# Performance work log

Hardware: AMD Instinct MI355X
Metric: run time of the kernel (lower is better)

The kernel has to match this reference:

```python
import jax, jax.numpy as jnp
import numpy as np

B, S, D_IN, D_OUT, H = 2, 2048, 1024, 1024, 16
DH = D_OUT // H


def setup_inputs() -> dict:
    key = jax.random.key(0)
    ks = jax.random.split(key, 6)
    sd_in = 1.0 / np.sqrt(D_IN)
    sd_out = 1.0 / np.sqrt(D_OUT)
    return {
        "x": jax.random.normal(ks[0], (B, S, D_IN), dtype=jnp.float32),
        "Wq": jax.random.uniform(ks[1], (D_IN, D_OUT), jnp.float32, -sd_in, sd_in),
        "Wk": jax.random.uniform(ks[2], (D_IN, D_OUT), jnp.float32, -sd_in, sd_in),
        "Wv": jax.random.uniform(ks[3], (D_IN, D_OUT), jnp.float32, -sd_in, sd_in),
        "Wo": jax.random.uniform(ks[4], (D_OUT, D_OUT), jnp.float32, -sd_out, sd_out),
        "bo": jax.random.uniform(ks[5], (D_OUT,), jnp.float32, -sd_out, sd_out),
    }


def reference(x, Wq, Wk, Wv, Wo, bo):
    b, n, _ = x.shape
    dh = DH
    # project and split heads: [b, n, d_out] -> [b, H, n, dh]
    def split(t):
        return t.reshape(b, n, H, dh).transpose(0, 2, 1, 3)
    q = split(x @ Wq)
    k = split(x @ Wk)
    v = split(x @ Wv)
    scores = jnp.einsum("bhqd,bhkd->bhqk", q, k)  # [b, H, n, n]
    causal = jnp.triu(jnp.ones((n, n), dtype=bool), k=1)
    scores = jnp.where(causal, -jnp.inf, scores)
    # NOTE: source scales by sqrt(num_tokens), not sqrt(d_head) — faithful.
    scale = 1.0 / (n ** 0.5)
    attn = jax.nn.softmax(scores * scale, axis=-1)
    ctx = jnp.einsum("bhqk,bhkd->bhqd", attn, v)  # [b, H, n, dh]
    ctx = ctx.transpose(0, 2, 1, 3).reshape(b, n, H * dh)
    return ctx @ Wo + bo
```

## Files before the change

### kernel.cpp

```cpp
#include <hip/hip_runtime.h>
#include <hip/hip_bf16.h>
#include <stdint.h>

#define B_   2
#define S_   2048
#define DIN  1024
#define DOUT 1024
#define H_   16
#define DH_  64

typedef __bf16 bf16_t;
typedef bf16_t bf16x8 __attribute__((ext_vector_type(8)));
typedef float  f32x4  __attribute__((ext_vector_type(4)));

#define WAITV(n) asm volatile("s_waitcnt vmcnt(" #n ")" ::: "memory")

static __device__ __forceinline__ void gld_lds16(const void* g, void* l) {
  __builtin_amdgcn_global_load_lds((const __attribute__((address_space(1))) void*)g,
                                   (__attribute__((address_space(3))) void*)l, 16, 0, 0);
}

static __device__ __forceinline__ unsigned short f2bf(float f) {
  __hip_bfloat16 h = __float2bfloat16(f);
  return __builtin_bit_cast(unsigned short, h);
}

static __device__ __forceinline__ float fexp2(float x) {
#if __has_builtin(__builtin_amdgcn_exp2f)
  return __builtin_amdgcn_exp2f(x);
#else
  return exp2f(x);
#endif
}

__global__ __launch_bounds__(256) void k_convert_x(const float* __restrict__ x,
                                                   unsigned short* __restrict__ xb) {
  int i = (blockIdx.x * 256 + threadIdx.x) * 4;
  float4 v = *reinterpret_cast<const float4*>(x + i);
  ushort4 o;
  o.x = f2bf(v.x); o.y = f2bf(v.y); o.z = f2bf(v.z); o.w = f2bf(v.w);
  *reinterpret_cast<ushort4*>(xb + i) = o;
}

__global__ __launch_bounds__(256) void k_transpose_w(const float* __restrict__ Wq,
                                                     const float* __restrict__ Wk,
                                                     const float* __restrict__ Wv,
                                                     const float* __restrict__ Wo,
                                                     __hip_bfloat16* __restrict__ Wt3,
                                                     __hip_bfloat16* __restrict__ Wot) {
  __shared__ float tile[32][33];
  const int z = blockIdx.z;
  const float* src = (z == 0) ? Wq : (z == 1) ? Wk : (z == 2) ? Wv : Wo;
  __hip_bfloat16* dst = (z < 3) ? (Wt3 + (size_t)z * DIN * DOUT) : Wot;
  const int n0 = blockIdx.x * 32, k0 = blockIdx.y * 32;
  const int tx = threadIdx.x, ty = threadIdx.y;
  #pragma unroll
  for (int i = ty; i < 32; i += 8)
    tile[i][tx] = src[(size_t)(k0 + i) * DOUT + n0 + tx];
  __syncthreads();
  #pragma unroll
  for (int i = ty; i < 32; i += 8)
    dst[(size_t)(n0 + i) * DIN + k0 + tx] = __float2bfloat16(tile[tx][i]);
}

template <int MODE, int TN>
__global__ __launch_bounds__(256) void k_gemm_bt(
    const __hip_bfloat16* __restrict__ A,
    const __hip_bfloat16* __restrict__ Bt,
    __hip_bfloat16* __restrict__ Qb, __hip_bfloat16* __restrict__ Kb,
    __hip_bfloat16* __restrict__ Vtb,
    float* __restrict__ Out, const float* __restrict__ bias,
    int M, int N, int K)
{
  constexpr int NFRAG = TN / 32;
  constexpr int LPT = 2 + TN / 64;
  __shared__ __align__(16) __hip_bfloat16 As[3][128 * 32];
  __shared__ __align__(16) __hip_bfloat16 Bs[3][TN * 32];
  const int tid = threadIdx.x;
  const int lane = tid & 63, wid = tid >> 6;
  const int r15 = lane & 15, g = lane >> 4;
  const int m0 = blockIdx.x * 128, n0 = blockIdx.y * TN;
  const int wr = wid >> 1, wc = wid & 1;
  f32x4 acc[4][NFRAG] = {};

  auto stage = [&](int bi, int kt) {
    #pragma unroll
    for (int i = 0; i < 2; ++i) {
      const int c = i * 256 + tid;
      const int row = c >> 2, kb = (c & 3) * 8;
      gld_lds16(A + (size_t)(m0 + row) * K + kt + kb, (void*)(As[bi] + (size_t)(c & ~63) * 8));
    }
    if constexpr (TN == 128) {
      #pragma unroll
      for (int i = 0; i < 2; ++i) {
        const int c = i * 256 + tid;
        const int row = c >> 2, kb = (c & 3) * 8;
        gld_lds16(Bt + (size_t)(n0 + row) * K + kt + kb, (void*)(Bs[bi] + (size_t)(c & ~63) * 8));
      }
    } else {
      const int c = tid;
      const int row = c >> 2, kb = (c & 3) * 8;
      gld_lds16(Bt + (size_t)(n0 + row) * K + kt + kb, (void*)(Bs[bi] + (size_t)(c & ~63) * 8));
    }
  };

  const int NT = K >> 5;
  stage(0, 0); stage(1, 32);
  if constexpr (TN == 128) WAITV(4); else WAITV(3);
  __builtin_amdgcn_s_barrier();

  int bi = 0;
  for (int t = 0; t < NT; ++t) {
    int bs = bi + 2; if (bs >= 3) bs -= 3;
    const bool st = (t + 2 < NT);
    if (st) stage(bs, (t + 2) * 32);
    bf16x8 af[4], bfr[NFRAG];
    #pragma unroll
    for (int mi = 0; mi < 4; ++mi)
      af[mi] = *reinterpret_cast<const bf16x8*>(As[bi] + (wr * 64 + mi * 16 + r15) * 32 + g * 8);
    #pragma unroll
    for (int ni = 0; ni < NFRAG; ++ni)
      bfr[ni] = *reinterpret_cast<const bf16x8*>(Bs[bi] + (wc * (TN / 2) + ni * 16 + r15) * 32 + g * 8);
    __builtin_amdgcn_s_setprio(1);
    #pragma unroll
    for (int mi = 0; mi < 4; ++mi)
      #pragma unroll
      for (int ni = 0; ni < NFRAG; ++ni)
        acc[mi][ni] = __builtin_amdgcn_mfma_f32_16x16x32_bf16(af[mi], bfr[ni], acc[mi][ni], 0, 0, 0);
    __builtin_amdgcn_s_setprio(0);
    if (t + 1 < NT) {
      if (st) { if constexpr (TN == 128) WAITV(4); else WAITV(3); }
      else    { WAITV(0); }
      __builtin_amdgcn_s_barrier();
    }
    bi = (bi + 1 == 3) ? 0 : bi + 1;
  }

  #pragma unroll
  for (int mi = 0; mi < 4; ++mi) {
    #pragma unroll
    for (int ni = 0; ni < NFRAG; ++ni) {
      const int mb = m0 + wr * 64 + mi * 16 + g * 4;
      const int n  = n0 + wc * (TN / 2) + ni * 16 + r15;
      if (MODE == 0) {
        const int w = n >> 10, nn = n & 1023;
        const int h = nn >> 6, dh = nn & 63;
        const int b = mb >> 11, s = mb & 2047;
        const size_t bh = (size_t)(b * H_ + h);
        if (w == 2) {
          ushort4 pv;
          pv.x = f2bf(acc[mi][ni][0]); pv.y = f2bf(acc[mi][ni][1]);
          pv.z = f2bf(acc[mi][ni][2]); pv.w = f2bf(acc[mi][ni][3]);
          *reinterpret_cast<ushort4*>((unsigned short*)Vtb + (bh * DH_ + dh) * S_ + s) = pv;
        } else {
          #pragma unroll
          for (int rr = 0; rr < 4; ++rr) {
            float v = acc[mi][ni][rr];
            if (w == 0) v *= 0.022097086912079608f * 1.4426950408889634f;
            const __hip_bfloat16 hv = __float2bfloat16(v);
            if (w == 0) Qb[(bh * S_ + s + rr) * DH_ + dh] = hv;
            else        Kb[(bh * S_ + s + rr) * DH_ + dh] = hv;
          }
        }
      } else {
        #pragma unroll
        for (int rr = 0; rr < 4; ++rr)
          Out[(size_t)(mb + rr) * N + n] = acc[mi][ni][rr] + bias[n];
      }
    }
  }
}

__global__ __launch_bounds__(256) void k_attn(
    const __hip_bfloat16* __restrict__ Qb,
    const __hip_bfloat16* __restrict__ Kb,
    const __hip_bfloat16* __restrict__ Vtb,
    __hip_bfloat16* __restrict__ Ctx)
{
  __shared__ __align__(16) __hip_bfloat16 Ks[2][64 * 64];
  __shared__ __align__(16) __hip_bfloat16 Vs[2][64 * 64];
  __shared__ __align__(16) unsigned short Pl[4][16 * 64];
  const int tid = threadIdx.x, lane = tid & 63, w = tid >> 6;
  const int r15 = lane & 15, g = lane >> 4;
  const int bh = blockIdx.x;
  const int b = bh >> 4, h = bh & 15;
  const int qb = 31 - blockIdx.y;
  const __hip_bfloat16* Qh = Qb  + (size_t)bh * S_ * DH_;
  const __hip_bfloat16* Kh = Kb  + (size_t)bh * S_ * DH_;
  const __hip_bfloat16* Vh = Vtb + (size_t)bh * DH_ * S_;
  char* PlW = (char*)&Pl[w][0];
  const int sw = (r15 & 7);
  const float FIXM = 4.0f;

  auto stage = [&](int bufi, int t) {
    const int kv0 = t * 64;
    #pragma unroll
    for (int i = 0; i < 2; ++i) {
      const int c = i * 256 + tid;
      const int r = c >> 3;
      const int scc = (c & 7) ^ (r & 7);
      const int cbase = i * 256 + w * 64;
      gld_lds16(Kh + (size_t)(kv0 + r) * DH_ + scc * 8, (void*)(Ks[bufi] + cbase * 8));
      gld_lds16(Vh + (size_t)r * S_ + kv0 + scc * 8,    (void*)(Vs[bufi] + cbase * 8));
    }
  };

  const int q = qb * 64 + w * 16 + r15;

  bf16x8 qf[2];
  #pragma unroll
  for (int ks = 0; ks < 2; ++ks)
    qf[ks] = *reinterpret_cast<const bf16x8*>(Qh + (size_t)q * DH_ + ks * 32 + g * 8);

  f32x4 of[4] = {};
  float lrow = 0.f;

  const int nt = qb + 1;
  stage(0, 0);
  __syncthreads();

  for (int t = 0; t < nt; ++t) {
    const int cur = t & 1;
    if (t + 1 < nt) stage(cur ^ 1, t + 1);
    const char* Kb_ = (const char*)Ks[cur];
    const char* Vb_ = (const char*)Vs[cur];
    const int kv0 = t * 64;

    f32x4 sf[4] = {};
    __builtin_amdgcn_s_setprio(1);
    #pragma unroll
    for (int ks = 0; ks < 2; ++ks)
      #pragma unroll
      for (int c = 0; c < 4; ++c) {
        bf16x8 kf = *reinterpret_cast<const bf16x8*>(
            Kb_ + (c * 16 + r15) * 128 + (((ks * 4 + g) ^ sw) * 16));
        sf[c] = __builtin_amdgcn_mfma_f32_16x16x32_bf16(kf, qf[ks], sf[c], 0, 0, 0);
      }
    __builtin_amdgcn_s_setprio(0);

    float pv[16];
    #pragma unroll
    for (int c = 0; c < 4; ++c)
      #pragma unroll
      for (int r = 0; r < 4; ++r)
        pv[c * 4 + r] = sf[c][r];
    if (t == qb) {
      #pragma unroll
      for (int c = 0; c < 4; ++c)
        #pragma unroll
        for (int r = 0; r < 4; ++r) {
          const int kv = kv0 + c * 16 + g * 4 + r;
          if (kv > q) pv[c * 4 + r] = -INFINITY;
        }
    }
    float pe[16];
    #pragma unroll
    for (int j = 0; j < 16; ++j) pe[j] = fexp2(pv[j] - FIXM);
    #pragma unroll
    for (int c = 0; c < 4; ++c) {
      ushort4 pw;
      pw.x = f2bf(pe[c * 4 + 0]); pw.y = f2bf(pe[c * 4 + 1]);
      pw.z = f2bf(pe[c * 4 + 2]); pw.w = f2bf(pe[c * 4 + 3]);
      const int chunk = (c * 2 + (g >> 1)) ^ sw;
      *reinterpret_cast<ushort4*>(PlW + r15 * 128 + chunk * 16 + (g & 1) * 8) = pw;
    }
    float s8[8], s4[4];
    #pragma unroll
    for (int j = 0; j < 8; ++j) s8[j] = pe[j] + pe[j + 8];
    #pragma unroll
    for (int j = 0; j < 4; ++j) s4[j] = s8[j] + s8[j + 4];
    lrow += (s4[0] + s4[1]) + (s4[2] + s4[3]);

    __builtin_amdgcn_s_setprio(1);
    #pragma unroll
    for (int ks = 0; ks < 2; ++ks) {
      bf16x8 pf = *reinterpret_cast<const bf16x8*>(
          PlW + r15 * 128 + (((ks * 4 + g) ^ sw) * 16));
      #pragma unroll
      for (int d = 0; d < 4; ++d) {
        bf16x8 vf = *reinterpret_cast<const bf16x8*>(
            Vb_ + (d * 16 + r15) * 128 + (((ks * 4 + g) ^ sw) * 16));
        of[d] = __builtin_amdgcn_mfma_f32_16x16x32_bf16(vf, pf, of[d], 0, 0, 0);
      }
    }
    __builtin_amdgcn_s_setprio(0);
    __syncthreads();
  }

  lrow += __shfl_xor(lrow, 16, 64);
  lrow += __shfl_xor(lrow, 32, 64);

  const float inv = 1.0f / lrow;
  unsigned short* Cp = (unsigned short*)Ctx + ((size_t)(b * S_ + q) * H_ + h) * DH_;
  #pragma unroll
  for (int d = 0; d < 4; ++d) {
    ushort4 ov;
    ov.x = f2bf(of[d][0] * inv); ov.y = f2bf(of[d][1] * inv);
    ov.z = f2bf(of[d][2] * inv); ov.w = f2bf(of[d][3] * inv);
    *reinterpret_cast<ushort4*>(Cp + d * 16 + g * 4) = ov;
  }
}

extern "C" void kernel_launch(void* const* d_in, const int* in_sizes, int n_in,
                              void* d_out, int out_size, void* d_ws, size_t ws_size,
                              hipStream_t stream) {
  const float* x  = (const float*)d_in[0];
  const float* Wq = (const float*)d_in[1];
  const float* Wk = (const float*)d_in[2];
  const float* Wv = (const float*)d_in[3];
  const float* Wo = (const float*)d_in[4];
  const float* bo = (const float*)d_in[5];
  float* out = (float*)d_out;

  uint8_t* ws = (uint8_t*)d_ws;
  __hip_bfloat16* xb  = (__hip_bfloat16*)(ws);
  __hip_bfloat16* Wt3 = (__hip_bfloat16*)(ws + 8388608);
  __hip_bfloat16* Wot = (__hip_bfloat16*)(ws + 14680064);
  __hip_bfloat16* Qb  = (__hip_bfloat16*)(ws + 16777216);
  __hip_bfloat16* Kb  = (__hip_bfloat16*)(ws + 25165824);
  __hip_bfloat16* Vtb = (__hip_bfloat16*)(ws + 33554432);
  __hip_bfloat16* Ctx = (__hip_bfloat16*)(ws + 41943040);

  k_convert_x<<<4096, 256, 0, stream>>>(x, (unsigned short*)xb);
  k_transpose_w<<<dim3(32, 32, 4), dim3(32, 8), 0, stream>>>(Wq, Wk, Wv, Wo, Wt3, Wot);
  k_gemm_bt<0, 128><<<dim3(32, 24), 256, 0, stream>>>(xb, Wt3, Qb, Kb, Vtb, nullptr, nullptr,
                                                      4096, 3072, 1024);
  k_attn<<<dim3(32, 32), 256, 0, stream>>>(Qb, Kb, Vtb, Ctx);
  k_gemm_bt<1, 64><<<dim3(32, 16), 256, 0, stream>>>(Ctx, Wot, nullptr, nullptr, nullptr,
                                                     out, bo, 4096, 1024, 1024);
}
```

Measured before the change: 108.2 us.

## Rewrite attention with 32x32x16 MFMA, 128-row query blocks and register-shuffled P

```diff
diff --git a/kernel.cpp b/kernel.cpp
--- a/kernel.cpp
+++ b/kernel.cpp
@@ -12,6 +12,9 @@
 typedef __bf16 bf16_t;
 typedef bf16_t bf16x8 __attribute__((ext_vector_type(8)));
 typedef float  f32x4  __attribute__((ext_vector_type(4)));
+typedef float  f32x16 __attribute__((ext_vector_type(16)));
+typedef unsigned int u32;
+typedef unsigned int u32x4 __attribute__((ext_vector_type(4)));
 
 #define WAITV(n) asm volatile("s_waitcnt vmcnt(" #n ")" ::: "memory")
 
@@ -73,7 +76,6 @@
     int M, int N, int K)
 {
   constexpr int NFRAG = TN / 32;
-  constexpr int LPT = 2 + TN / 64;
   __shared__ __align__(16) __hip_bfloat16 As[3][128 * 32];
   __shared__ __align__(16) __hip_bfloat16 Bs[3][TN * 32];
   const int tid = threadIdx.x;
@@ -179,17 +181,17 @@
 {
   __shared__ __align__(16) __hip_bfloat16 Ks[2][64 * 64];
   __shared__ __align__(16) __hip_bfloat16 Vs[2][64 * 64];
-  __shared__ __align__(16) unsigned short Pl[4][16 * 64];
   const int tid = threadIdx.x, lane = tid & 63, w = tid >> 6;
-  const int r15 = lane & 15, g = lane >> 4;
+  const int l31 = lane & 31, l5 = lane >> 5;
   const int bh = blockIdx.x;
   const int b = bh >> 4, h = bh & 15;
-  const int qb = 31 - blockIdx.y;
+  const int byy = 15 - blockIdx.y;
+  const int q0 = byy * 128;
+  const int q0w = q0 + w * 32;
+  const int q = q0w + l31;
   const __hip_bfloat16* Qh = Qb  + (size_t)bh * S_ * DH_;
   const __hip_bfloat16* Kh = Kb  + (size_t)bh * S_ * DH_;
   const __hip_bfloat16* Vh = Vtb + (size_t)bh * DH_ * S_;
-  char* PlW = (char*)&Pl[w][0];
-  const int sw = (r15 & 7);
   const float FIXM = 4.0f;
 
   auto stage = [&](int bufi, int t) {
@@ -205,100 +207,117 @@
     }
   };
 
-  const int q = qb * 64 + w * 16 + r15;
-
-  bf16x8 qf[2];
-  #pragma unroll
-  for (int ks = 0; ks < 2; ++ks)
-    qf[ks] = *reinterpret_cast<const bf16x8*>(Qh + (size_t)q * DH_ + ks * 32 + g * 8);
-
-  f32x4 of[4] = {};
-  float lrow = 0.f;
-
-  const int nt = qb + 1;
+  bf16x8 qf[4];
+  #pragma unroll
+  for (int kf = 0; kf < 4; ++kf)
+    qf[kf] = *reinterpret_cast<const bf16x8*>(Qh + (size_t)q * DH_ + kf * 16 + l5 * 8);
+
+  f32x16 of[2] = {};
+  float lsum = 0.f;
+
+  const int nt = 2 * byy + 2;
   stage(0, 0);
   __syncthreads();
 
   for (int t = 0; t < nt; ++t) {
     const int cur = t & 1;
     if (t + 1 < nt) stage(cur ^ 1, t + 1);
-    const char* Kb_ = (const char*)Ks[cur];
-    const char* Vb_ = (const char*)Vs[cur];
+    const char* Kp = (const char*)Ks[cur];
+    const char* Vp = (const char*)Vs[cur];
     const int kv0 = t * 64;
 
-    f32x4 sf[4] = {};
-    __builtin_amdgcn_s_setprio(1);
-    #pragma unroll
-    for (int ks = 0; ks < 2; ++ks)
-      #pragma unroll
-      for (int c = 0; c < 4; ++c) {
-        bf16x8 kf = *reinterpret_cast<const bf16x8*>(
-            Kb_ + (c * 16 + r15) * 128 + (((ks * 4 + g) ^ sw) * 16));
-        sf[c] = __builtin_amdgcn_mfma_f32_16x16x32_bf16(kf, qf[ks], sf[c], 0, 0, 0);
+    if (kv0 <= q0w + 31) {
+      f32x16 sf[2] = {};
+      __builtin_amdgcn_s_setprio(1);
+      #pragma unroll
+      for (int kf = 0; kf < 4; ++kf)
+        #pragma unroll
+        for (int kvf = 0; kvf < 2; ++kvf) {
+          const int row = kvf * 32 + l31;
+          bf16x8 kfrag = *reinterpret_cast<const bf16x8*>(
+              Kp + row * 128 + (((kf * 2 + l5) ^ (row & 7)) * 16));
+          sf[kvf] = __builtin_amdgcn_mfma_f32_32x32x16_bf16(kfrag, qf[kf], sf[kvf], 0, 0, 0);
+        }
+      __builtin_amdgcn_s_setprio(0);
+
+      const bool diag = (kv0 + 64 > q0w);
+      u32 Apk[2][8];
+      #pragma unroll
+      for (int kvf = 0; kvf < 2; ++kvf) {
+        float pe[16];
+        #pragma unroll
+        for (int reg = 0; reg < 16; ++reg) {
+          const int rowo = (reg & 3) + 8 * (reg >> 2) + 4 * l5;
+          float v = sf[kvf][reg];
+          if (diag) {
+            const int kvg = kv0 + kvf * 32 + rowo;
+            if (kvg > q) v = -INFINITY;
+          }
+          pe[reg] = fexp2(v - FIXM);
+        }
+        float s2[8], s4[4];
+        #pragma unroll
+        for (int i = 0; i < 8; ++i) s2[i] = pe[2 * i] + pe[2 * i + 1];
+        #pragma unroll
+        for (int i = 0; i < 4; ++i) s4[i] = s2[2 * i] + s2[2 * i + 1];
+        lsum += (s4[0] + s4[1]) + (s4[2] + s4[3]);
+        #pragma unroll
+        for (int i = 0; i < 8; ++i)
+          Apk[kvf][i] = (u32)f2bf(pe[2 * i]) | ((u32)f2bf(pe[2 * i + 1]) << 16);
       }
-    __builtin_amdgcn_s_setprio(0);
-
-    float pv[16];
-    #pragma unroll
-    for (int c = 0; c < 4; ++c)
-      #pragma unroll
-      for (int r = 0; r < 4; ++r)
-        pv[c * 4 + r] = sf[c][r];
-    if (t == qb) {
-      #pragma unroll
-      for (int c = 0; c < 4; ++c)
-        #pragma unroll
-        for (int r = 0; r < 4; ++r) {
-          const int kv = kv0 + c * 16 + g * 4 + r;
-          if (kv > q) pv[c * 4 + r] = -INFINITY;
+      u32 Xp[2][8];
+      #pragma unroll
+      for (int kvf = 0; kvf < 2; ++kvf)
+        #pragma unroll
+        for (int i = 0; i < 8; ++i)
+          Xp[kvf][i] = (u32)__shfl_xor((int)Apk[kvf][i], 32, 64);
+
+      bf16x8 pfr[4];
+      #pragma unroll
+      for (int kvf = 0; kvf < 2; ++kvf) {
+        u32x4 e, o;
+        e.x = l5 ? Xp[kvf][2] : Apk[kvf][0];
+        e.y = l5 ? Xp[kvf][3] : Apk[kvf][1];
+        e.z = l5 ? Apk[kvf][2] : Xp[kvf][0];
+        e.w = l5 ? Apk[kvf][3] : Xp[kvf][1];
+        o.x = l5 ? Xp[kvf][6] : Apk[kvf][4];
+        o.y = l5 ? Xp[kvf][7] : Apk[kvf][5];
+        o.z = l5 ? Apk[kvf][6] : Xp[kvf][4];
+        o.w = l5 ? Apk[kvf][7] : Xp[kvf][5];
+        pfr[kvf * 2]     = __builtin_bit_cast(bf16x8, e);
+        pfr[kvf * 2 + 1] = __builtin_bit_cast(bf16x8, o);
+      }
+
+      __builtin_amdgcn_s_setprio(1);
+      #pragma unroll
+      for (int kvf2 = 0; kvf2 < 4; ++kvf2)
+        #pragma unroll
+        for (int dhf = 0; dhf < 2; ++dhf) {
+          const int row = dhf * 32 + l31;
+          bf16x8 vfrag = *reinterpret_cast<const bf16x8*>(
+              Vp + row * 128 + (((kvf2 * 2 + l5) ^ (row & 7)) * 16));
+          of[dhf] = __builtin_amdgcn_mfma_f32_32x32x16_bf16(vfrag, pfr[kvf2], of[dhf], 0, 0, 0);
         }
-    }
-    float pe[16];
-    #pragma unroll
-    for (int j = 0; j < 16; ++j) pe[j] = fexp2(pv[j] - FIXM);
-    #pragma unroll
-    for (int c = 0; c < 4; ++c) {
-      ushort4 pw;
-      pw.x = f2bf(pe[c * 4 + 0]); pw.y = f2bf(pe[c * 4 + 1]);
-      pw.z = f2bf(pe[c * 4 + 2]); pw.w = f2bf(pe[c * 4 + 3]);
-      const int chunk = (c * 2 + (g >> 1)) ^ sw;
-      *reinterpret_cast<ushort4*>(PlW + r15 * 128 + chunk * 16 + (g & 1) * 8) = pw;
-    }
-    float s8[8], s4[4];
-    #pragma unroll
-    for (int j = 0; j < 8; ++j) s8[j] = pe[j] + pe[j + 8];
-    #pragma unroll
-    for (int j = 0; j < 4; ++j) s4[j] = s8[j] + s8[j + 4];
-    lrow += (s4[0] + s4[1]) + (s4[2] + s4[3]);
-
-    __builtin_amdgcn_s_setprio(1);
-    #pragma unroll
-    for (int ks = 0; ks < 2; ++ks) {
-      bf16x8 pf = *reinterpret_cast<const bf16x8*>(
-          PlW + r15 * 128 + (((ks * 4 + g) ^ sw) * 16));
-      #pragma unroll
-      for (int d = 0; d < 4; ++d) {
-        bf16x8 vf = *reinterpret_cast<const bf16x8*>(
-            Vb_ + (d * 16 + r15) * 128 + (((ks * 4 + g) ^ sw) * 16));
-        of[d] = __builtin_amdgcn_mfma_f32_16x16x32_bf16(vf, pf, of[d], 0, 0, 0);
-      }
-    }
-    __builtin_amdgcn_s_setprio(0);
+      __builtin_amdgcn_s_setprio(0);
+    }
     __syncthreads();
   }
 
-  lrow += __shfl_xor(lrow, 16, 64);
-  lrow += __shfl_xor(lrow, 32, 64);
-
-  const float inv = 1.0f / lrow;
+  lsum += __shfl_xor(lsum, 32, 64);
+  const float inv = 1.0f / lsum;
+
   unsigned short* Cp = (unsigned short*)Ctx + ((size_t)(b * S_ + q) * H_ + h) * DH_;
   #pragma unroll
-  for (int d = 0; d < 4; ++d) {
-    ushort4 ov;
-    ov.x = f2bf(of[d][0] * inv); ov.y = f2bf(of[d][1] * inv);
-    ov.z = f2bf(of[d][2] * inv); ov.w = f2bf(of[d][3] * inv);
-    *reinterpret_cast<ushort4*>(Cp + d * 16 + g * 4) = ov;
-  }
+  for (int dhf = 0; dhf < 2; ++dhf)
+    #pragma unroll
+    for (int rg = 0; rg < 4; ++rg) {
+      ushort4 ov;
+      ov.x = f2bf(of[dhf][rg * 4 + 0] * inv);
+      ov.y = f2bf(of[dhf][rg * 4 + 1] * inv);
+      ov.z = f2bf(of[dhf][rg * 4 + 2] * inv);
+      ov.w = f2bf(of[dhf][rg * 4 + 3] * inv);
+      *reinterpret_cast<ushort4*>(Cp + dhf * 32 + rg * 8 + l5 * 4) = ov;
+    }
 }
 
 extern "C" void kernel_launch(void* const* d_in, const int* in_sizes, int n_in,
@@ -325,7 +344,7 @@
   k_transpose_w<<<dim3(32, 32, 4), dim3(32, 8), 0, stream>>>(Wq, Wk, Wv, Wo, Wt3, Wot);
   k_gemm_bt<0, 128><<<dim3(32, 24), 256, 0, stream>>>(xb, Wt3, Qb, Kb, Vtb, nullptr, nullptr,
                                                       4096, 3072, 1024);
-  k_attn<<<dim3(32, 32), 256, 0, stream>>>(Qb, Kb, Vtb, Ctx);
+  k_attn<<<dim3(32, 16), 256, 0, stream>>>(Qb, Kb, Vtb, Ctx);
   k_gemm_bt<1, 64><<<dim3(32, 16), 256, 0, stream>>>(Ctx, Wot, nullptr, nullptr, nullptr,
                                                      out, bo, 4096, 1024, 1024);
 }
```

After: 138.0 us. 27.6% more time.

## Process two 16-row query fragments per wave in attention, doubling Q tile to 128

Applied to the files above, without the earlier changes.

```diff
diff --git a/kernel.cpp b/kernel.cpp
--- a/kernel.cpp
+++ b/kernel.cpp
@@ -73,7 +73,6 @@
     int M, int N, int K)
 {
   constexpr int NFRAG = TN / 32;
-  constexpr int LPT = 2 + TN / 64;
   __shared__ __align__(16) __hip_bfloat16 As[3][128 * 32];
   __shared__ __align__(16) __hip_bfloat16 Bs[3][TN * 32];
   const int tid = threadIdx.x;
@@ -179,16 +178,19 @@
 {
   __shared__ __align__(16) __hip_bfloat16 Ks[2][64 * 64];
   __shared__ __align__(16) __hip_bfloat16 Vs[2][64 * 64];
-  __shared__ __align__(16) unsigned short Pl[4][16 * 64];
+  __shared__ __align__(16) unsigned short Pl[4][2][16 * 64];
   const int tid = threadIdx.x, lane = tid & 63, w = tid >> 6;
   const int r15 = lane & 15, g = lane >> 4;
   const int bh = blockIdx.x;
   const int b = bh >> 4, h = bh & 15;
-  const int qb = 31 - blockIdx.y;
+  const int byy = 15 - blockIdx.y;
+  const int q0w = byy * 128 + w * 32;
+  const int qA = q0w + r15, qB = q0w + 16 + r15;
   const __hip_bfloat16* Qh = Qb  + (size_t)bh * S_ * DH_;
   const __hip_bfloat16* Kh = Kb  + (size_t)bh * S_ * DH_;
   const __hip_bfloat16* Vh = Vtb + (size_t)bh * DH_ * S_;
-  char* PlW = (char*)&Pl[w][0];
+  char* PlA = (char*)&Pl[w][0][0];
+  char* PlB = (char*)&Pl[w][1][0];
   const int sw = (r15 & 7);
   const float FIXM = 4.0f;
 
@@ -205,17 +207,17 @@
     }
   };
 
-  const int q = qb * 64 + w * 16 + r15;
-
-  bf16x8 qf[2];
-  #pragma unroll
-  for (int ks = 0; ks < 2; ++ks)
-    qf[ks] = *reinterpret_cast<const bf16x8*>(Qh + (size_t)q * DH_ + ks * 32 + g * 8);
-
-  f32x4 of[4] = {};
-  float lrow = 0.f;
-
-  const int nt = qb + 1;
+  bf16x8 qfr[2][2];
+  #pragma unroll
+  for (int ks = 0; ks < 2; ++ks) {
+    qfr[0][ks] = *reinterpret_cast<const bf16x8*>(Qh + (size_t)qA * DH_ + ks * 32 + g * 8);
+    qfr[1][ks] = *reinterpret_cast<const bf16x8*>(Qh + (size_t)qB * DH_ + ks * 32 + g * 8);
+  }
+
+  f32x4 ofA[4] = {}, ofB[4] = {};
+  float lrowA = 0.f, lrowB = 0.f;
+
+  const int nt = 2 * byy + 2;
   stage(0, 0);
   __syncthreads();
 
@@ -225,79 +227,110 @@
     const char* Kb_ = (const char*)Ks[cur];
     const char* Vb_ = (const char*)Vs[cur];
     const int kv0 = t * 64;
-
-    f32x4 sf[4] = {};
-    __builtin_amdgcn_s_setprio(1);
-    #pragma unroll
-    for (int ks = 0; ks < 2; ++ks)
-      #pragma unroll
-      for (int c = 0; c < 4; ++c) {
-        bf16x8 kf = *reinterpret_cast<const bf16x8*>(
-            Kb_ + (c * 16 + r15) * 128 + (((ks * 4 + g) ^ sw) * 16));
-        sf[c] = __builtin_amdgcn_mfma_f32_16x16x32_bf16(kf, qf[ks], sf[c], 0, 0, 0);
+    const bool actB = (kv0 <= q0w + 31);
+    const bool actA = (kv0 <= q0w + 15);
+
+    if (actB) {
+      bf16x8 kf[2][4];
+      #pragma unroll
+      for (int ks = 0; ks < 2; ++ks)
+        #pragma unroll
+        for (int c = 0; c < 4; ++c)
+          kf[ks][c] = *reinterpret_cast<const bf16x8*>(
+              Kb_ + (c * 16 + r15) * 128 + (((ks * 4 + g) ^ sw) * 16));
+
+      f32x4 sfA[4] = {}, sfB[4] = {};
+      __builtin_amdgcn_s_setprio(1);
+      #pragma unroll
+      for (int ks = 0; ks < 2; ++ks)
+        #pragma unroll
+        for (int c = 0; c < 4; ++c) {
+          if (actA)
+            sfA[c] = __builtin_amdgcn_mfma_f32_16x16x32_bf16(kf[ks][c], qfr[0][ks], sfA[c], 0, 0, 0);
+          sfB[c] = __builtin_amdgcn_mfma_f32_16x16x32_bf16(kf[ks][c], qfr[1][ks], sfB[c], 0, 0, 0);
+        }
+      __builtin_amdgcn_s_setprio(0);
+
+      #pragma unroll
+      for (int qf = 0; qf < 2; ++qf) {
+        if (qf == 0 && !actA) continue;
+        f32x4* sf = (qf == 0) ? sfA : sfB;
+        char* PlW = (qf == 0) ? PlA : PlB;
+        const int q = (qf == 0) ? qA : qB;
+        float pv[16];
+        #pragma unroll
+        for (int c = 0; c < 4; ++c)
+          #pragma unroll
+          for (int r = 0; r < 4; ++r)
+            pv[c * 4 + r] = sf[c][r];
+        if (kv0 + 64 > q0w + qf * 16) {
+          #pragma unroll
+          for (int c = 0; c < 4; ++c)
+            #pragma unroll
+            for (int r = 0; r < 4; ++r) {
+              const int kv = kv0 + c * 16 + g * 4 + r;
+              if (kv > q) pv[c * 4 + r] = -INFINITY;
+            }
+        }
+        float pe[16];
+        #pragma unroll
+        for (int j = 0; j < 16; ++j) pe[j] = fexp2(pv[j] - FIXM);
+        #pragma unroll
+        for (int c = 0; c < 4; ++c) {
+          ushort4 pw;
+          pw.x = f2bf(pe[c * 4 + 0]); pw.y = f2bf(pe[c * 4 + 1]);
+          pw.z = f2bf(pe[c * 4 + 2]); pw.w = f2bf(pe[c * 4 + 3]);
+          const int chunk = (c * 2 + (g >> 1)) ^ sw;
+          *reinterpret_cast<ushort4*>(PlW + r15 * 128 + chunk * 16 + (g & 1) * 8) = pw;
+        }
+        float s8[8], s4[4];
+        #pragma unroll
+        for (int j = 0; j < 8; ++j) s8[j] = pe[j] + pe[j + 8];
+        #pragma unroll
+        for (int j = 0; j < 4; ++j) s4[j] = s8[j] + s8[j + 4];
+        const float ps = (s4[0] + s4[1]) + (s4[2] + s4[3]);
+        if (qf == 0) lrowA += ps; else lrowB += ps;
       }
-    __builtin_amdgcn_s_setprio(0);
-
-    float pv[16];
-    #pragma unroll
-    for (int c = 0; c < 4; ++c)
-      #pragma unroll
-      for (int r = 0; r < 4; ++r)
-        pv[c * 4 + r] = sf[c][r];
-    if (t == qb) {
-      #pragma unroll
-      for (int c = 0; c < 4; ++c)
-        #pragma unroll
-        for (int r = 0; r < 4; ++r) {
-          const int kv = kv0 + c * 16 + g * 4 + r;
-          if (kv > q) pv[c * 4 + r] = -INFINITY;
-        }
-    }
-    float pe[16];
-    #pragma unroll
-    for (int j = 0; j < 16; ++j) pe[j] = fexp2(pv[j] - FIXM);
-    #pragma unroll
-    for (int c = 0; c < 4; ++c) {
-      ushort4 pw;
-      pw.x = f2bf(pe[c * 4 + 0]); pw.y = f2bf(pe[c * 4 + 1]);
-      pw.z = f2bf(pe[c * 4 + 2]); pw.w = f2bf(pe[c * 4 + 3]);
-      const int chunk = (c * 2 + (g >> 1)) ^ sw;
-      *reinterpret_cast<ushort4*>(PlW + r15 * 128 + chunk * 16 + (g & 1) * 8) = pw;
-    }
-    float s8[8], s4[4];
-    #pragma unroll
-    for (int j = 0; j < 8; ++j) s8[j] = pe[j] + pe[j + 8];
-    #pragma unroll
-    for (int j = 0; j < 4; ++j) s4[j] = s8[j] + s8[j + 4];
-    lrow += (s4[0] + s4[1]) + (s4[2] + s4[3]);
-
-    __builtin_amdgcn_s_setprio(1);
-    #pragma unroll
-    for (int ks = 0; ks < 2; ++ks) {
-      bf16x8 pf = *reinterpret_cast<const bf16x8*>(
-          PlW + r15 * 128 + (((ks * 4 + g) ^ sw) * 16));
-      #pragma unroll
-      for (int d = 0; d < 4; ++d) {
-        bf16x8 vf = *reinterpret_cast<const bf16x8*>(
-            Vb_ + (d * 16 + r15) * 128 + (((ks * 4 + g) ^ sw) * 16));
-        of[d] = __builtin_amdgcn_mfma_f32_16x16x32_bf16(vf, pf, of[d], 0, 0, 0);
+
+      __builtin_amdgcn_s_setprio(1);
+      #pragma unroll
+      for (int ks = 0; ks < 2; ++ks) {
+        bf16x8 pfA = *reinterpret_cast<const bf16x8*>(
+            PlA + r15 * 128 + (((ks * 4 + g) ^ sw) * 16));
+        bf16x8 pfB = *reinterpret_cast<const bf16x8*>(
+            PlB + r15 * 128 + (((ks * 4 + g) ^ sw) * 16));
+        #pragma unroll
+        for (int d = 0; d < 4; ++d) {
+          bf16x8 vf = *reinterpret_cast<const bf16x8*>(
+              Vb_ + (d * 16 + r15) * 128 + (((ks * 4 + g) ^ sw) * 16));
+          if (actA)
+            ofA[d] = __builtin_amdgcn_mfma_f32_16x16x32_bf16(vf, pfA, ofA[d], 0, 0, 0);
+          ofB[d] = __builtin_amdgcn_mfma_f32_16x16x32_bf16(vf, pfB, ofB[d], 0, 0, 0);
+        }
       }
-    }
-    __builtin_amdgcn_s_setprio(0);
+      __builtin_amdgcn_s_setprio(0);
+    }
     __syncthreads();
   }
 
-  lrow += __shfl_xor(lrow, 16, 64);
-  lrow += __shfl_xor(lrow, 32, 64);
-
-  const float inv = 1.0f / lrow;
-  unsigned short* Cp = (unsigned short*)Ctx + ((size_t)(b * S_ + q) * H_ + h) * DH_;
+  lrowA += __shfl_xor(lrowA, 16, 64);
+  lrowA += __shfl_xor(lrowA, 32, 64);
+  lrowB += __shfl_xor(lrowB, 16, 64);
+  lrowB += __shfl_xor(lrowB, 32, 64);
+
+  const float invA = 1.0f / lrowA, invB = 1.0f / lrowB;
+  unsigned short* CpA = (unsigned short*)Ctx + ((size_t)(b * S_ + qA) * H_ + h) * DH_;
+  unsigned short* CpB = (unsigned short*)Ctx + ((size_t)(b * S_ + qB) * H_ + h) * DH_;
   #pragma unroll
   for (int d = 0; d < 4; ++d) {
     ushort4 ov;
-    ov.x = f2bf(of[d][0] * inv); ov.y = f2bf(of[d][1] * inv);
-    ov.z = f2bf(of[d][2] * inv); ov.w = f2bf(of[d][3] * inv);
-    *reinterpret_cast<ushort4*>(Cp + d * 16 + g * 4) = ov;
+    ov.x = f2bf(ofA[d][0] * invA); ov.y = f2bf(ofA[d][1] * invA);
+    ov.z = f2bf(ofA[d][2] * invA); ov.w = f2bf(ofA[d][3] * invA);
+    *reinterpret_cast<ushort4*>(CpA + d * 16 + g * 4) = ov;
+    ushort4 ow;
+    ow.x = f2bf(ofB[d][0] * invB); ow.y = f2bf(ofB[d][1] * invB);
+    ow.z = f2bf(ofB[d][2] * invB); ow.w = f2bf(ofB[d][3] * invB);
+    *reinterpret_cast<ushort4*>(CpB + d * 16 + g * 4) = ow;
   }
 }
 
@@ -325,7 +358,7 @@
   k_transpose_w<<<dim3(32, 32, 4), dim3(32, 8), 0, stream>>>(Wq, Wk, Wv, Wo, Wt3, Wot);
   k_gemm_bt<0, 128><<<dim3(32, 24), 256, 0, stream>>>(xb, Wt3, Qb, Kb, Vtb, nullptr, nullptr,
                                                       4096, 3072, 1024);
-  k_attn<<<dim3(32, 32), 256, 0, stream>>>(Qb, Kb, Vtb, Ctx);
+  k_attn<<<dim3(32, 16), 256, 0, stream>>>(Qb, Kb, Vtb, Ctx);
   k_gemm_bt<1, 64><<<dim3(32, 16), 256, 0, stream>>>(Ctx, Wot, nullptr, nullptr, nullptr,
                                                      out, bo, 4096, 1024, 1024);
 }
```

Result: slower. 131.2 us (+21.3%).
